# Kernel tuning notes

Hardware: AMD Instinct MI355X
Metric: run time of the kernel (lower is better)

Reference implementation:

```python
import jax, jax.numpy as jnp
import numpy as np

B, N1, N2, C2, K = 8, 2048, 128, 256, 3
D_POS, H0, H1 = 32, 512, 1024


def setup_inputs() -> dict:
    key = jax.random.key(0)
    ks = jax.random.split(key, 14)
    return {
        "xyz1": jax.random.normal(ks[0], (B, N1, 3), jnp.float32),
        "xyz2": jax.random.normal(ks[1], (B, N2, 3), jnp.float32),
        "feat2": jax.random.normal(ks[2], (B, N2, C2), jnp.float32),
        "lrf2": jax.random.normal(ks[3], (B, N2, 3, 3), jnp.float32),
        "w_pos": jax.random.normal(ks[4], (D_POS, 4), jnp.float32) * 0.1,
        "pos_scale": jax.random.uniform(ks[5], (D_POS,), jnp.float32, 0.5, 1.5),
        "pos_bias": jax.random.normal(ks[6], (D_POS,), jnp.float32) * 0.1,
        "w0": jax.random.normal(ks[7], (H0, C2 + D_POS), jnp.float32) * 0.05,
        "s0": jax.random.uniform(ks[8], (H0,), jnp.float32, 0.5, 1.5),
        "b0": jax.random.normal(ks[9], (H0,), jnp.float32) * 0.1,
        "w1": jax.random.normal(ks[10], (H1, H0), jnp.float32) * 0.04,
        "s1": jax.random.uniform(ks[11], (H1,), jnp.float32, 0.5, 1.5),
        "b1": jax.random.normal(ks[12], (H1,), jnp.float32) * 0.1,
        "k": K,
    }


def reference(xyz1, xyz2, feat2, lrf2, w_pos, pos_scale, pos_bias,
              w0, s0, b0, w1, s1, b1, k):
    Bb = xyz1.shape[0]
    # --- get_dists: full pairwise sqrt-distance matrix (B, N1, N2) ---
    d2 = (jnp.sum(xyz1 * xyz1, -1)[:, :, None]
          + jnp.sum(xyz2 * xyz2, -1)[:, None, :]
          - 2.0 * jnp.einsum('bmc,bnc->bmn', xyz1, xyz2))
    dists = jnp.sqrt(jnp.where(d2 < 0, 1e-7, d2))
    # --- k-NN: smallest k in ascending order (== torch.sort then slice) ---
    _, inds = jax.lax.top_k(-dists, k)                    # (B, N1, k)
    bidx = jnp.arange(Bb)[:, None, None]
    feat_nb = feat2[bidx, inds]                           # (B, N1, k, C2)
    close = xyz2[bidx, inds]                              # (B, N1, k, 3)
    lrf_nb = lrf2[bidx, inds]                             # (B, N1, k, 3, 3)
    # --- geometric angle embedding ---
    rel = xyz1[:, :, None, :] - close                     # (B, N1, k, 3)
    rel_norm = jnp.linalg.norm(rel, axis=-1)              # (B, N1, k)
    unit = rel / jnp.maximum(rel_norm, 1e-12)[..., None]  # F.normalize eps
    angle = jnp.einsum('bnkij,bnkj->bnki', lrf_nb, unit)  # (B, N1, k, 3)
    rp = jnp.concatenate([rel_norm[..., None], angle], -1)  # (B, N1, k, 4)
    # --- posembed: 1x1 Conv2d (no bias) + folded BN + LeakyReLU(0.2) ---
    pos = jax.nn.leaky_relu(
        jnp.einsum('bnkc,oc->bnko', rp, w_pos) * pos_scale + pos_bias, 0.2)
    # --- backbone: two 1x1 convs with folded BN + ReLU ---
    x = jnp.concatenate([feat_nb, pos], -1)               # (B, N1, k, C2+32)
    h0 = jax.nn.relu(jnp.einsum('bnkc,oc->bnko', x, w0) * s0 + b0)
    h1 = jax.nn.relu(jnp.einsum('bnkc,oc->bnko', h0, w1) * s1 + b1)
    # --- sum over neighbors, return (B, C_out, N1) like torch ---
    return jnp.transpose(jnp.sum(h1, axis=2), (0, 2, 1))
```

## Files before the change

### kernel.cpp

```cpp
#include <hip/hip_runtime.h>


typedef unsigned short u16;
typedef __bf16 bf16x8 __attribute__((ext_vector_type(8)));
typedef float f32x4 __attribute__((ext_vector_type(4)));
typedef u16 u16x4 __attribute__((ext_vector_type(4)));
typedef u16 u16x8 __attribute__((ext_vector_type(8)));

#define BQ 8
#define N1Q 2048
#define N2Q 128
#define C2Q 256
#define DPOS 32
#define H0Q 512
#define H1Q 1024
#define NQ (BQ * N1Q)

#define WS_W0F 0u
#define WS_W0P 262144u
#define WS_W1 294912u
#define WS_F2B 1343488u
#define WS_F 1867776u
#define WS_H0 3964928u
#define WS_POS 54296576u
#define WS_IDX 57442304u

__device__ __forceinline__ u16 f2bf(float f) {
  unsigned int u = __builtin_bit_cast(unsigned int, f);
  return (u16)((u + 0x7FFFu + ((u >> 16) & 1u)) >> 16);
}

__device__ __forceinline__ void load16_lds(const void* g, void* l) {
  __builtin_amdgcn_global_load_lds(
      (const __attribute__((address_space(1))) unsigned int*)g,
      (__attribute__((address_space(3))) unsigned int*)l, 16, 0, 0);
}

__global__ __launch_bounds__(512, 2) void prep(
    const float* __restrict__ xyz1, const float* __restrict__ xyz2,
    const float* __restrict__ lrf2, const float* __restrict__ w_pos,
    const float* __restrict__ pscale, const float* __restrict__ pbias,
    const float* __restrict__ w0, const float* __restrict__ w1,
    const float* __restrict__ feat2,
    u16* __restrict__ posw, int* __restrict__ idxw,
    u16* __restrict__ w0f, u16* __restrict__ w0p,
    u16* __restrict__ w1b, u16* __restrict__ f2b) {
  if (blockIdx.x >= 128) {
    int i = (blockIdx.x - 128) * 512 + threadIdx.x;
    if (i < 131072) {
      int h = i >> 8, c = i & 255;
      w0f[i] = f2bf(w0[h * 288 + c]);
    } else if (i < 147456) {
      int j = i - 131072;
      int h = j >> 5, c = j & 31;
      w0p[j] = f2bf(w0[h * 288 + 256 + c]);
    } else if (i < 671744) {
      int j = i - 147456;
      w1b[j] = f2bf(w1[j]);
    } else {
      int j = i - 671744;
      f2b[j] = f2bf(feat2[j]);
    }
    return;
  }

  __shared__ float xyz2s[N2Q * 3];
  __shared__ float n2s[N2Q];
  __shared__ float lrfs[N2Q * 9];
  __shared__ float wps[DPOS * 4];
  __shared__ float pss[DPOS];
  __shared__ float pbs[DPOS];
  __shared__ float candd[128 * 13];
  __shared__ int candi[128 * 13];
  __shared__ int idxb[384];

  const int t = threadIdx.x;
  const int qb = blockIdx.x * 128;
  const int b = qb >> 11;

  for (int i = t; i < N2Q * 3; i += 512) xyz2s[i] = xyz2[b * N2Q * 3 + i];
  for (int i = t; i < N2Q * 9; i += 512) lrfs[i] = lrf2[b * N2Q * 9 + i];
  if (t < DPOS * 4) wps[t] = w_pos[t];
  if (t < DPOS) { pss[t] = pscale[t]; pbs[t] = pbias[t]; }
  __syncthreads();
  if (t < N2Q) {
    float x = xyz2s[t * 3], y = xyz2s[t * 3 + 1], z = xyz2s[t * 3 + 2];
    n2s[t] = x * x + y * y + z * z;
  }
  __syncthreads();

  {
    const int ql = t >> 2, qt = t & 3;
    const int q = qb + ql;
    const float px = xyz1[q * 3], py = xyz1[q * 3 + 1], pz = xyz1[q * 3 + 2];
    const float pn = px * px + py * py + pz * pz;
    float d0 = 1e30f, d1 = 1e30f, d2v = 1e30f;
    int i0 = 0, i1 = 0, i2 = 0;
    const int ibeg = qt * 32;
    for (int i = ibeg; i < ibeg + 32; i++) {
      float dt = px * xyz2s[i * 3] + py * xyz2s[i * 3 + 1] + pz * xyz2s[i * 3 + 2];
      float d = pn + n2s[i] - 2.f * dt;
      if (d < d0) {
        d2v = d1; i2 = i1; d1 = d0; i1 = i0; d0 = d; i0 = i;
      } else if (d < d1) {
        d2v = d1; i2 = i1; d1 = d; i1 = i;
      } else if (d < d2v) {
        d2v = d; i2 = i;
      }
    }
    int base = ql * 13 + qt * 3;
    candd[base] = d0;      candi[base] = i0;
    candd[base + 1] = d1;  candi[base + 1] = i1;
    candd[base + 2] = d2v; candi[base + 2] = i2;
  }
  __syncthreads();

  if (t < 128) {
    float d0 = 1e30f, d1 = 1e30f, d2v = 1e30f;
    int i0 = 0, i1 = 0, i2 = 0;
    int base = t * 13;
#pragma unroll
    for (int c = 0; c < 12; c++) {
      float d = candd[base + c];
      int id = candi[base + c];
      if (d < d0) {
        d2v = d1; i2 = i1; d1 = d0; i1 = i0; d0 = d; i0 = id;
      } else if (d < d1) {
        d2v = d1; i2 = i1; d1 = d; i1 = id;
      } else if (d < d2v) {
        d2v = d; i2 = id;
      }
    }
    idxb[t] = i0;
    idxb[128 + t] = i1;
    idxb[256 + t] = i2;
  }
  __syncthreads();

  if (t < 384) {
    const int j = t >> 7, ql = t & 127;
    const int q = qb + ql;
    const float px = xyz1[q * 3], py = xyz1[q * 3 + 1], pz = xyz1[q * 3 + 2];
    const int id = idxb[j * 128 + ql];
    float rx = px - xyz2s[id * 3];
    float ry = py - xyz2s[id * 3 + 1];
    float rz = pz - xyz2s[id * 3 + 2];
    float rn = sqrtf(rx * rx + ry * ry + rz * rz);
    float inv = 1.f / fmaxf(rn, 1e-12f);
    float ux = rx * inv, uy = ry * inv, uz = rz * inv;
    const float* L = lrfs + id * 9;
    float a0 = L[0] * ux + L[1] * uy + L[2] * uz;
    float a1 = L[3] * ux + L[4] * uy + L[5] * uz;
    float a2 = L[6] * ux + L[7] * uy + L[8] * uz;
    const size_t row = (size_t)j * NQ + q;
    idxw[row] = id;
#pragma unroll
    for (int c = 0; c < 4; c++) {
      u16x8 chunk;
#pragma unroll
      for (int e = 0; e < 8; e++) {
        int o = c * 8 + e;
        float v = wps[o * 4] * rn + wps[o * 4 + 1] * a0 + wps[o * 4 + 2] * a1 +
                  wps[o * 4 + 3] * a2;
        v = v * pss[o] + pbs[o];
        v = (v >= 0.f) ? v : 0.2f * v;
        chunk[e] = f2bf(v);
      }
      *(u16x8*)(posw + row * 32 + c * 8) = chunk;
    }
  }
}

__global__ __launch_bounds__(256, 2) void fgemm(const u16* __restrict__ A,
                                                const u16* __restrict__ W,
                                                float* __restrict__ F) {
  __shared__ alignas(16) u16 As[128 * 32];
  __shared__ alignas(16) u16 Bs[128 * 32];
  const int m0 = (blockIdx.x >> 2) * 128, n0 = (blockIdx.x & 3) * 128;
  const int t = threadIdx.x;
  const int wv = t >> 6, lane = t & 63;
  const int wm = wv >> 1, wn = wv & 1;
  const int quad = lane >> 4, cc = lane & 15;
  const int srow = lane & 15, skc = quad * 8;
  f32x4 acc[4][4] = {};

  for (int k0 = 0; k0 < 256; k0 += 32) {
#pragma unroll
    for (int i = 0; i < 2; i++) {
      int g = i * 4 + wv;
      load16_lds(A + (size_t)(m0 + g * 16 + srow) * 256 + k0 + skc,
                 (char*)As + g * 1024 + (lane << 4));
      load16_lds(W + (size_t)(n0 + g * 16 + srow) * 256 + k0 + skc,
                 (char*)Bs + g * 1024 + (lane << 4));
    }
    __syncthreads();
    bf16x8 af[4], bf[4];
#pragma unroll
    for (int mt = 0; mt < 4; mt++)
      af[mt] = *(const bf16x8*)((const char*)As + (wm * 4 + mt) * 1024 + (lane << 4));
#pragma unroll
    for (int nt = 0; nt < 4; nt++)
      bf[nt] = *(const bf16x8*)((const char*)Bs + (wn * 4 + nt) * 1024 + (lane << 4));
#pragma unroll
    for (int mt = 0; mt < 4; mt++)
#pragma unroll
      for (int nt = 0; nt < 4; nt++)
        acc[mt][nt] = __builtin_amdgcn_mfma_f32_16x16x32_bf16(
            af[mt], bf[nt], acc[mt][nt], 0, 0, 0);
    __syncthreads();
  }

#pragma unroll
  for (int nt = 0; nt < 4; nt++) {
    int gn = n0 + wn * 64 + nt * 16 + cc;
#pragma unroll
    for (int mt = 0; mt < 4; mt++) {
      int gm = m0 + wm * 64 + mt * 16 + quad * 4;
#pragma unroll
      for (int r = 0; r < 4; r++)
        F[(size_t)(gm + r) * H0Q + gn] = acc[mt][nt][r];
    }
  }
}

__global__ __launch_bounds__(256, 4) void h0_kernel(
    const u16* __restrict__ posw, const int* __restrict__ idxw,
    const u16* __restrict__ w0p, const float* __restrict__ F,
    const float* __restrict__ s0, const float* __restrict__ b0,
    u16* __restrict__ H0) {
  const int t = threadIdx.x;
  const int wv = t >> 6, lane = t & 63;
  const int quad = lane >> 4, cc = lane & 15;
  const int r0 = (blockIdx.x * 4 + wv) * 16;

  const int r = r0 + cc;
  const int q = r & (NQ - 1);
  const int bb = q >> 11;
  const int idv = idxw[r];
  const float* Fr = F + ((size_t)(bb * N2Q + idv)) * H0Q;
  u16* Hr = H0 + (size_t)r * H0Q;

  const bf16x8 afr = *(const bf16x8*)(posw + (size_t)r * 32 + quad * 8);
  const f32x4 zf = {};

#pragma unroll 4
  for (int nt = 0; nt < 32; nt++) {
    const bf16x8 bfr = *(const bf16x8*)(w0p + (nt * 16 + cc) * 32 + quad * 8);
    f32x4 acc = __builtin_amdgcn_mfma_f32_16x16x32_bf16(bfr, afr, zf, 0, 0, 0);
    const int hb = nt * 16 + quad * 4;
    const f32x4 sv = *(const f32x4*)(s0 + hb);
    const f32x4 bv = *(const f32x4*)(b0 + hb);
    const f32x4 fv = *(const f32x4*)(Fr + hb);
    u16x4 o4;
#pragma unroll
    for (int e = 0; e < 4; e++) {
      float h = (fv[e] + acc[e]) * sv[e] + bv[e];
      h = h > 0.f ? h : 0.f;
      o4[e] = f2bf(h);
    }
    *(u16x4*)(Hr + hb) = o4;
  }
}

__global__ __launch_bounds__(512, 2) void gemm2(const u16* __restrict__ A,
                                                const u16* __restrict__ W,
                                                const float* __restrict__ s,
                                                const float* __restrict__ bz,
                                                float* __restrict__ out) {
  __shared__ alignas(16) char smem[3][40960];
  const int id = blockIdx.x;
  const int xcd = id & 7, g = id >> 3;
  const int m0 = (xcd * 16 + (g >> 2)) * 128;
  const int n0 = (g & 3) * 256;
  const int t = threadIdx.x;
  const int wv = t >> 6, lane = t & 63;
  const int wm = wv >> 2, wn = wv & 3;
  const int quad = lane >> 4, cc = lane & 15;
  const int lr = lane & 15, lk = quad * 8;

  const size_t aOff = (size_t)(m0 + wv * 16 + lr) * 512 + lk;
  size_t bOff[2];
#pragma unroll
  for (int i = 0; i < 2; i++)
    bOff[i] = (size_t)(n0 + (wv * 2 + i) * 16 + lr) * 512 + lk;

  auto stage = [&](int kt, int buf) {
    const int k0 = kt << 5;
    char* dst = smem[buf] + (lane << 4);
#pragma unroll
    for (int j = 0; j < 3; j++)
      load16_lds(A + (size_t)j * NQ * H0Q + aOff + k0,
                 dst + j * 8192 + wv * 1024);
#pragma unroll
    for (int i = 0; i < 2; i++)
      load16_lds(W + bOff[i] + k0, dst + 24576 + (wv * 2 + i) * 1024);
  };

  f32x4 acc[3][4][4] = {};

  stage(0, 0);
  stage(1, 1);

  int bi = 0, sb = 2;
  for (int kt = 0; kt < 16; kt++) {
    if (kt < 15)
      asm volatile("s_waitcnt vmcnt(5)" ::: "memory");
    else
      asm volatile("s_waitcnt vmcnt(0)" ::: "memory");
    __builtin_amdgcn_s_barrier();
    if (kt + 2 < 16) {
      stage(kt + 2, sb);
      sb = (sb == 2) ? 0 : sb + 1;
    }
    const char* base = smem[bi] + (lane << 4);
    bf16x8 bf[4];
#pragma unroll
    for (int nt = 0; nt < 4; nt++)
      bf[nt] = *(const bf16x8*)(base + 24576 + (wn * 4 + nt) * 1024);
#pragma unroll
    for (int j = 0; j < 3; j++) {
      bf16x8 af[4];
#pragma unroll
      for (int mt = 0; mt < 4; mt++)
        af[mt] = *(const bf16x8*)(base + j * 8192 + (wm * 4 + mt) * 1024);
      __builtin_amdgcn_s_setprio(1);
#pragma unroll
      for (int mt = 0; mt < 4; mt++)
#pragma unroll
        for (int nt = 0; nt < 4; nt++)
          acc[j][mt][nt] = __builtin_amdgcn_mfma_f32_16x16x32_bf16(
              af[mt], bf[nt], acc[j][mt][nt], 0, 0, 0);
      __builtin_amdgcn_s_setprio(0);
    }
    bi = (bi == 2) ? 0 : bi + 1;
  }

#pragma unroll
  for (int nt = 0; nt < 4; nt++) {
    int gn = n0 + wn * 64 + nt * 16 + cc;
    float sv = s[gn], bv = bz[gn];
#pragma unroll
    for (int mt = 0; mt < 4; mt++) {
      int gm = m0 + wm * 64 + mt * 16 + quad * 4;
#pragma unroll
      for (int r = 0; r < 4; r++) {
        float h0v = acc[0][mt][nt][r] * sv + bv;
        float h1v = acc[1][mt][nt][r] * sv + bv;
        float h2v = acc[2][mt][nt][r] * sv + bv;
        float v = (h0v > 0.f ? h0v : 0.f) + (h1v > 0.f ? h1v : 0.f) +
                  (h2v > 0.f ? h2v : 0.f);
        int q = gm + r;
        out[((size_t)(q >> 11) * H1Q + gn) * N1Q + (q & 2047)] = v;
      }
    }
  }
}

extern "C" void kernel_launch(void* const* d_in, const int* in_sizes, int n_in,
                              void* d_out, int out_size, void* d_ws,
                              size_t ws_size, hipStream_t stream) {
  const float* xyz1 = (const float*)d_in[0];
  const float* xyz2 = (const float*)d_in[1];
  const float* feat2 = (const float*)d_in[2];
  const float* lrf2 = (const float*)d_in[3];
  const float* w_pos = (const float*)d_in[4];
  const float* pscale = (const float*)d_in[5];
  const float* pbias = (const float*)d_in[6];
  const float* w0 = (const float*)d_in[7];
  const float* s0 = (const float*)d_in[8];
  const float* b0 = (const float*)d_in[9];
  const float* w1 = (const float*)d_in[10];
  const float* s1 = (const float*)d_in[11];
  const float* b1 = (const float*)d_in[12];
  float* out = (float*)d_out;

  char* ws = (char*)d_ws;
  u16* w0f = (u16*)(ws + WS_W0F);
  u16* w0p = (u16*)(ws + WS_W0P);
  u16* w1b = (u16*)(ws + WS_W1);
  u16* f2b = (u16*)(ws + WS_F2B);
  float* F = (float*)(ws + WS_F);
  u16* H0 = (u16*)(ws + WS_H0);
  u16* posw = (u16*)(ws + WS_POS);
  int* idxw = (int*)(ws + WS_IDX);

  prep<<<1952, 512, 0, stream>>>(xyz1, xyz2, lrf2, w_pos, pscale, pbias, w0,
                                 w1, feat2, posw, idxw, w0f, w0p, w1b, f2b);
  fgemm<<<32, 256, 0, stream>>>(f2b, w0f, F);
  h0_kernel<<<768, 256, 0, stream>>>(posw, idxw, w0p, F, s0, b0, H0);
  gemm2<<<512, 512, 0, stream>>>(H0, w1b, s1, b1, out);
}
```

Measured before the change: 201.6 us.

## Fuse prep, feature GEMM and h0 stage into one cooperative kernel

Merges the preprocessing, the per-source feature GEMM and the H0 construction into a single cooperative kernel of 256 blocks, using a grid-wide sync between the F computation and its gathered use. The feature GEMM now converts fp32 feat2 and w0 to bf16 on the fly inside each wave, which drops the separate bf16 copies of feat2 and w0f and their kernels. This removes two launches and some conversion traffic. In exchange it adds a grid barrier and a small one-wave-per-tile GEMM with non-vectorized loads, and the h0 work now runs on only 256 blocks.

```diff
diff --git a/kernel.cpp b/kernel.cpp
--- a/kernel.cpp
+++ b/kernel.cpp
@@ -1,5 +1,8 @@
 #include <hip/hip_runtime.h>
-
+#include <hip/hip_cooperative_groups.h>
+
+
+namespace cg = cooperative_groups;
 
 typedef unsigned short u16;
 typedef __bf16 bf16x8 __attribute__((ext_vector_type(8)));
@@ -16,10 +19,8 @@
 #define H1Q 1024
 #define NQ (BQ * N1Q)
 
-#define WS_W0F 0u
 #define WS_W0P 262144u
 #define WS_W1 294912u
-#define WS_F2B 1343488u
 #define WS_F 1867776u
 #define WS_H0 3964928u
 #define WS_POS 54296576u
@@ -36,48 +37,48 @@
       (__attribute__((address_space(3))) unsigned int*)l, 16, 0, 0);
 }
 
-__global__ __launch_bounds__(512, 2) void prep(
+__global__ __launch_bounds__(512, 2) void pre3(
     const float* __restrict__ xyz1, const float* __restrict__ xyz2,
     const float* __restrict__ lrf2, const float* __restrict__ w_pos,
     const float* __restrict__ pscale, const float* __restrict__ pbias,
     const float* __restrict__ w0, const float* __restrict__ w1,
-    const float* __restrict__ feat2,
-    u16* __restrict__ posw, int* __restrict__ idxw,
-    u16* __restrict__ w0f, u16* __restrict__ w0p,
-    u16* __restrict__ w1b, u16* __restrict__ f2b) {
-  if (blockIdx.x >= 128) {
-    int i = (blockIdx.x - 128) * 512 + threadIdx.x;
-    if (i < 131072) {
-      int h = i >> 8, c = i & 255;
-      w0f[i] = f2bf(w0[h * 288 + c]);
-    } else if (i < 147456) {
-      int j = i - 131072;
-      int h = j >> 5, c = j & 31;
-      w0p[j] = f2bf(w0[h * 288 + 256 + c]);
-    } else if (i < 671744) {
-      int j = i - 147456;
-      w1b[j] = f2bf(w1[j]);
-    } else {
-      int j = i - 671744;
-      f2b[j] = f2bf(feat2[j]);
-    }
-    return;
-  }
-
+    const float* __restrict__ feat2, const float* __restrict__ s0,
+    const float* __restrict__ b0, u16* __restrict__ posw,
+    int* __restrict__ idxw, u16* __restrict__ w0p, u16* __restrict__ w1b,
+    float* __restrict__ F, u16* __restrict__ H0) {
   __shared__ float xyz2s[N2Q * 3];
   __shared__ float n2s[N2Q];
   __shared__ float lrfs[N2Q * 9];
   __shared__ float wps[DPOS * 4];
   __shared__ float pss[DPOS];
   __shared__ float pbs[DPOS];
-  __shared__ float candd[128 * 13];
-  __shared__ int candi[128 * 13];
-  __shared__ int idxb[384];
+  __shared__ float candd[64 * 13];
+  __shared__ int candi[64 * 13];
+  __shared__ int idxb[192];
 
   const int t = threadIdx.x;
-  const int qb = blockIdx.x * 128;
+  const int wv = t >> 6, lane = t & 63;
+  const int quad = lane >> 4, cc = lane & 15;
+
+  {
+    const int gtid = blockIdx.x * 512 + t;
+    for (int j = gtid; j < 135168; j += 131072) {
+      if (j < 131072) {
+        f32x4 v = *(const f32x4*)(w1 + (size_t)j * 4);
+        u16x4 o = {f2bf(v[0]), f2bf(v[1]), f2bf(v[2]), f2bf(v[3])};
+        *(u16x4*)(w1b + (size_t)j * 4) = o;
+      } else {
+        int k = j - 131072;
+        int h = k >> 3, c4 = k & 7;
+        f32x4 v = *(const f32x4*)(w0 + h * 288 + 256 + c4 * 4);
+        u16x4 o = {f2bf(v[0]), f2bf(v[1]), f2bf(v[2]), f2bf(v[3])};
+        *(u16x4*)(w0p + h * 32 + c4 * 4) = o;
+      }
+    }
+  }
+
+  const int qb = blockIdx.x * 64;
   const int b = qb >> 11;
-
   for (int i = t; i < N2Q * 3; i += 512) xyz2s[i] = xyz2[b * N2Q * 3 + i];
   for (int i = t; i < N2Q * 9; i += 512) lrfs[i] = lrf2[b * N2Q * 9 + i];
   if (t < DPOS * 4) wps[t] = w_pos[t];
@@ -89,7 +90,7 @@
   }
   __syncthreads();
 
-  {
+  if (t < 256) {
     const int ql = t >> 2, qt = t & 3;
     const int q = qb + ql;
     const float px = xyz1[q * 3], py = xyz1[q * 3 + 1], pz = xyz1[q * 3 + 2];
@@ -115,7 +116,7 @@
   }
   __syncthreads();
 
-  if (t < 128) {
+  if (t < 64) {
     float d0 = 1e30f, d1 = 1e30f, d2v = 1e30f;
     int i0 = 0, i1 = 0, i2 = 0;
     int base = t * 13;
@@ -132,16 +133,16 @@
       }
     }
     idxb[t] = i0;
-    idxb[128 + t] = i1;
-    idxb[256 + t] = i2;
+    idxb[64 + t] = i1;
+    idxb[128 + t] = i2;
   }
   __syncthreads();
 
-  if (t < 384) {
-    const int j = t >> 7, ql = t & 127;
+  if (t < 192) {
+    const int j = t >> 6, ql = t & 63;
     const int q = qb + ql;
     const float px = xyz1[q * 3], py = xyz1[q * 3 + 1], pz = xyz1[q * 3 + 2];
-    const int id = idxb[j * 128 + ql];
+    const int id = idxb[t];
     float rx = px - xyz2s[id * 3];
     float ry = py - xyz2s[id * 3 + 1];
     float rz = pz - xyz2s[id * 3 + 2];
@@ -169,96 +170,64 @@
       *(u16x8*)(posw + row * 32 + c * 8) = chunk;
     }
   }
-}
-
-__global__ __launch_bounds__(256, 2) void fgemm(const u16* __restrict__ A,
-                                                const u16* __restrict__ W,
-                                                float* __restrict__ F) {
-  __shared__ alignas(16) u16 As[128 * 32];
-  __shared__ alignas(16) u16 Bs[128 * 32];
-  const int m0 = (blockIdx.x >> 2) * 128, n0 = (blockIdx.x & 3) * 128;
-  const int t = threadIdx.x;
-  const int wv = t >> 6, lane = t & 63;
-  const int wm = wv >> 1, wn = wv & 1;
-  const int quad = lane >> 4, cc = lane & 15;
-  const int srow = lane & 15, skc = quad * 8;
-  f32x4 acc[4][4] = {};
-
-  for (int k0 = 0; k0 < 256; k0 += 32) {
-#pragma unroll
-    for (int i = 0; i < 2; i++) {
-      int g = i * 4 + wv;
-      load16_lds(A + (size_t)(m0 + g * 16 + srow) * 256 + k0 + skc,
-                 (char*)As + g * 1024 + (lane << 4));
-      load16_lds(W + (size_t)(n0 + g * 16 + srow) * 256 + k0 + skc,
-                 (char*)Bs + g * 1024 + (lane << 4));
-    }
-    __syncthreads();
-    bf16x8 af[4], bf[4];
-#pragma unroll
-    for (int mt = 0; mt < 4; mt++)
-      af[mt] = *(const bf16x8*)((const char*)As + (wm * 4 + mt) * 1024 + (lane << 4));
-#pragma unroll
-    for (int nt = 0; nt < 4; nt++)
-      bf[nt] = *(const bf16x8*)((const char*)Bs + (wn * 4 + nt) * 1024 + (lane << 4));
-#pragma unroll
-    for (int mt = 0; mt < 4; mt++)
-#pragma unroll
-      for (int nt = 0; nt < 4; nt++)
-        acc[mt][nt] = __builtin_amdgcn_mfma_f32_16x16x32_bf16(
-            af[mt], bf[nt], acc[mt][nt], 0, 0, 0);
-    __syncthreads();
-  }
-
-#pragma unroll
-  for (int nt = 0; nt < 4; nt++) {
-    int gn = n0 + wn * 64 + nt * 16 + cc;
-#pragma unroll
-    for (int mt = 0; mt < 4; mt++) {
-      int gm = m0 + wm * 64 + mt * 16 + quad * 4;
-#pragma unroll
-      for (int r = 0; r < 4; r++)
-        F[(size_t)(gm + r) * H0Q + gn] = acc[mt][nt][r];
-    }
-  }
-}
-
-__global__ __launch_bounds__(256, 4) void h0_kernel(
-    const u16* __restrict__ posw, const int* __restrict__ idxw,
-    const u16* __restrict__ w0p, const float* __restrict__ F,
-    const float* __restrict__ s0, const float* __restrict__ b0,
-    u16* __restrict__ H0) {
-  const int t = threadIdx.x;
-  const int wv = t >> 6, lane = t & 63;
-  const int quad = lane >> 4, cc = lane & 15;
-  const int r0 = (blockIdx.x * 4 + wv) * 16;
-
-  const int r = r0 + cc;
-  const int q = r & (NQ - 1);
-  const int bb = q >> 11;
-  const int idv = idxw[r];
-  const float* Fr = F + ((size_t)(bb * N2Q + idv)) * H0Q;
-  u16* Hr = H0 + (size_t)r * H0Q;
-
-  const bf16x8 afr = *(const bf16x8*)(posw + (size_t)r * 32 + quad * 8);
-  const f32x4 zf = {};
-
+
+  {
+    const int wid = blockIdx.x * 8 + wv;
+    const int m0 = (wid >> 5) * 16;
+    const int n0 = (wid & 31) * 16;
+    const float* fa0 = feat2 + (size_t)(m0 + cc) * 256 + quad * 8;
+    const float* fb0 = w0 + (size_t)(n0 + cc) * 288 + quad * 8;
+    f32x4 acc = {};
+#pragma unroll
+    for (int q8 = 0; q8 < 8; q8++) {
+      u16x8 au, bu;
+#pragma unroll
+      for (int e = 0; e < 8; e++) {
+        au[e] = f2bf(fa0[q8 * 32 + e]);
+        bu[e] = f2bf(fb0[q8 * 32 + e]);
+      }
+      acc = __builtin_amdgcn_mfma_f32_16x16x32_bf16(
+          __builtin_bit_cast(bf16x8, au), __builtin_bit_cast(bf16x8, bu), acc,
+          0, 0, 0);
+    }
+#pragma unroll
+    for (int r = 0; r < 4; r++)
+      F[(size_t)(m0 + quad * 4 + r) * H0Q + n0 + cc] = acc[r];
+  }
+
+  cg::this_grid().sync();
+
+  {
+    const int wid = blockIdx.x * 8 + wv;
+    for (int u = wid; u < 3072; u += 2048) {
+      const int r = u * 16 + cc;
+      const int q = r & (NQ - 1);
+      const int bb = q >> 11;
+      const int idv = idxw[r];
+      const float* Fr = F + ((size_t)(bb * N2Q + idv)) * H0Q;
+      u16* Hr = H0 + (size_t)r * H0Q;
+      const bf16x8 afr = *(const bf16x8*)(posw + (size_t)r * 32 + quad * 8);
+      const f32x4 zf = {};
 #pragma unroll 4
-  for (int nt = 0; nt < 32; nt++) {
-    const bf16x8 bfr = *(const bf16x8*)(w0p + (nt * 16 + cc) * 32 + quad * 8);
-    f32x4 acc = __builtin_amdgcn_mfma_f32_16x16x32_bf16(bfr, afr, zf, 0, 0, 0);
-    const int hb = nt * 16 + quad * 4;
-    const f32x4 sv = *(const f32x4*)(s0 + hb);
-    const f32x4 bv = *(const f32x4*)(b0 + hb);
-    const f32x4 fv = *(const f32x4*)(Fr + hb);
-    u16x4 o4;
-#pragma unroll
-    for (int e = 0; e < 4; e++) {
-      float h = (fv[e] + acc[e]) * sv[e] + bv[e];
-      h = h > 0.f ? h : 0.f;
-      o4[e] = f2bf(h);
-    }
-    *(u16x4*)(Hr + hb) = o4;
+      for (int nt = 0; nt < 32; nt++) {
+        const bf16x8 bfr =
+            *(const bf16x8*)(w0p + (nt * 16 + cc) * 32 + quad * 8);
+        f32x4 acc =
+            __builtin_amdgcn_mfma_f32_16x16x32_bf16(bfr, afr, zf, 0, 0, 0);
+        const int hb = nt * 16 + quad * 4;
+        const f32x4 sv = *(const f32x4*)(s0 + hb);
+        const f32x4 bv = *(const f32x4*)(b0 + hb);
+        const f32x4 fv = *(const f32x4*)(Fr + hb);
+        u16x4 o4;
+#pragma unroll
+        for (int e = 0; e < 4; e++) {
+          float h = (fv[e] + acc[e]) * sv[e] + bv[e];
+          h = h > 0.f ? h : 0.f;
+          o4[e] = f2bf(h);
+        }
+        *(u16x4*)(Hr + hb) = o4;
+      }
+    }
   }
 }
 
@@ -375,18 +344,17 @@
   float* out = (float*)d_out;
 
   char* ws = (char*)d_ws;
-  u16* w0f = (u16*)(ws + WS_W0F);
   u16* w0p = (u16*)(ws + WS_W0P);
   u16* w1b = (u16*)(ws + WS_W1);
-  u16* f2b = (u16*)(ws + WS_F2B);
   float* F = (float*)(ws + WS_F);
   u16* H0 = (u16*)(ws + WS_H0);
   u16* posw = (u16*)(ws + WS_POS);
   int* idxw = (int*)(ws + WS_IDX);
 
-  prep<<<1952, 512, 0, stream>>>(xyz1, xyz2, lrf2, w_pos, pscale, pbias, w0,
-                                 w1, feat2, posw, idxw, w0f, w0p, w1b, f2b);
-  fgemm<<<32, 256, 0, stream>>>(f2b, w0f, F);
-  h0_kernel<<<768, 256, 0, stream>>>(posw, idxw, w0p, F, s0, b0, H0);
+  void* args[] = {&xyz1, &xyz2,  &lrf2, &w_pos, &pscale, &pbias,
+                  &w0,   &w1,    &feat2, &s0,   &b0,     &posw,
+                  &idxw, &w0p,   &w1b,  &F,     &H0};
+  hipLaunchCooperativeKernel((void*)pre3, dim3(256), dim3(512), args, 0,
+                             stream);
   gemm2<<<512, 512, 0, stream>>>(H0, w1b, s1, b1, out);
 }
```

Result: slower. 253.6 us (+25.8%).
